# Kernel optimization log

Measured on AMD Instinct MI355X. Metric: run time of the kernel, lower is better.

## Reference

```python
import jax, jax.numpy as jnp
import numpy as np

B, N, DIM, HID = 128, 4096, 16, 128

def _linear_init(key, fan_in, fan_out):
    # torch nn.Linear default: U(-1/sqrt(fan_in), 1/sqrt(fan_in))
    kw, kb = jax.random.split(key)
    bound = 1.0 / np.sqrt(fan_in)
    W = jax.random.uniform(kw, (fan_in, fan_out), minval=-bound, maxval=bound, dtype=jnp.float32)
    b = jax.random.uniform(kb, (fan_out,), minval=-bound, maxval=bound, dtype=jnp.float32)
    return W, b

def setup_inputs() -> dict:
    key = jax.random.key(0)
    ks = jax.random.split(key, 8)
    x = jax.random.normal(ks[0], (B, N, DIM), dtype=jnp.float32)
    adj_col = (jax.random.uniform(ks[1], (N,), dtype=jnp.float32) > 0.5).astype(jnp.float32)
    W_n2e, b_n2e = _linear_init(ks[2], 2 * DIM, HID)
    W_e2e, b_e2e = _linear_init(ks[3], HID, HID)
    W_e2n, b_e2n = _linear_init(ks[4], HID, HID)
    W_n2n, b_n2n = _linear_init(ks[5], HID, HID)
    W_out, b_out = _linear_init(ks[6], DIM + HID, DIM)
    return {"x": x, "adj_col": adj_col,
            "W_n2e": W_n2e, "b_n2e": b_n2e,
            "W_e2e": W_e2e, "b_e2e": b_e2e,
            "W_e2n": W_e2n, "b_e2n": b_e2n,
            "W_n2n": W_n2n, "b_n2n": b_n2n,
            "W_out": W_out, "b_out": b_out,
            "i": 0}

def reference(x, adj_col, W_n2e, b_n2e, W_e2e, b_e2e, W_e2n, b_e2n, W_n2n, b_n2n, W_out, b_out, i):
    starter = x                                        # [B, N, dim]
    ender = x[:, i, :][:, None, :]                     # [B, 1, dim]
    ender = jnp.broadcast_to(ender, starter.shape)     # [B, N, dim]
    h = jnp.concatenate([starter, ender], axis=2)      # [B, N, 2*dim]
    h = jax.nn.relu(h @ W_n2e + b_n2e)                 # [B, N, hid]
    h = jax.nn.relu(h @ W_e2e + b_e2e)                 # [B, N, hid]
    h = h * adj_col[None, :, None]                     # adjacency mask
    h = jnp.sum(h, axis=1)                             # [B, hid]
    h = jax.nn.relu(h @ W_e2n + b_e2n)
    h = jax.nn.relu(h @ W_n2n + b_n2n)
    h = jnp.concatenate([starter[:, i, :], h], axis=-1)  # [B, dim+hid]
    return h @ W_out + b_out                           # [B, dim]
```

## Files before the change

### kernel.cpp

```cpp
#include <hip/hip_runtime.h>
#include <hip/hip_bf16.h>

#define B_    128
#define N_    4096
#define DIM_  16
#define HID_  128
#define NT_   2
#define ROWS_ (N_ / NT_)

typedef __bf16 bf16x2 __attribute__((ext_vector_type(2)));
typedef __bf16 bf16x8 __attribute__((ext_vector_type(8)));
typedef float floatx16 __attribute__((ext_vector_type(16)));
typedef unsigned int u32;
typedef unsigned int u32x4 __attribute__((ext_vector_type(4)));

__device__ inline bf16x8 load_cvt8(const float* __restrict__ p) {
  const float4 u = *(const float4*)p;
  const float4 v = *(const float4*)(p + 4);
  bf16x8 r;
  r[0] = (__bf16)u.x; r[1] = (__bf16)u.y; r[2] = (__bf16)u.z; r[3] = (__bf16)u.w;
  r[4] = (__bf16)v.x; r[5] = (__bf16)v.y; r[6] = (__bf16)v.z; r[7] = (__bf16)v.w;
  return r;
}

__device__ inline u32 pk2(float a, float b) {
  bf16x2 p; p[0] = (__bf16)a; p[1] = (__bf16)b;
  return __builtin_bit_cast(u32, p);
}

__global__ __launch_bounds__(256, 2) void edge_kernel(
    const float* __restrict__ x, const float* __restrict__ adj,
    const float* __restrict__ W1, const float* __restrict__ b1,
    const float* __restrict__ W2, const float* __restrict__ b2,
    const int* __restrict__ ip, float* __restrict__ part)
{
  __shared__ __align__(16) __bf16 sW2[HID_ * HID_];
  __shared__ int   sIdx[ROWS_ + 32];
  __shared__ float sAcc[HID_];
  __shared__ float sB1[HID_];
  __shared__ float sEnder[DIM_];
  __shared__ int   sCnt;

  const int t  = threadIdx.x;
  const int b  = blockIdx.y;
  const int n0 = blockIdx.x * ROWS_;
  const int ii = __ldg(ip);

  const int wave = t >> 6, lane = t & 63;
  const int half = lane >> 5, l31 = lane & 31;

  if (t == 0) sCnt = 0;
  if (t < HID_) sAcc[t] = 0.f;
  if (t < DIM_) sEnder[t] = x[((size_t)b * N_ + ii) * DIM_ + t];
  __syncthreads();

  #pragma unroll
  for (int r = t; r < ROWS_; r += 256) {
    const bool act = adj[n0 + r] != 0.f;
    const unsigned long long m = __ballot(act);
    int base = 0;
    if (lane == 0) base = atomicAdd(&sCnt, __popcll(m));
    base = __shfl(base, 0);
    if (act) {
      const int pre = __builtin_amdgcn_mbcnt_hi((u32)(m >> 32),
                      __builtin_amdgcn_mbcnt_lo((u32)m, 0));
      sIdx[base + pre] = n0 + r;
    }
  }

  #pragma unroll
  for (int e = 0; e < 8; ++e) {
    const int G = t * 8 + e;
    const int c = G >> 4, g = G & 15;
    bf16x8 v;
    #pragma unroll
    for (int j = 0; j < 8; ++j) v[j] = (__bf16)W2[((g << 3) + j) * HID_ + c];
    *(bf16x8*)&sW2[(c << 7) + ((g ^ (c & 15)) << 3)] = v;
  }

  bf16x8 w1f[4];
  #pragma unroll
  for (int ft = 0; ft < 4; ++ft) {
    bf16x8 v;
    #pragma unroll
    for (int j = 0; j < 8; ++j)
      v[j] = (__bf16)W1[(half * 8 + j) * HID_ + (ft * 32 + l31)];
    w1f[ft] = v;
  }

  if (t < HID_) {
    float s = b1[t];
    #pragma unroll
    for (int k = 0; k < DIM_; ++k) s += sEnder[k] * W1[(DIM_ + k) * HID_ + t];
    sB1[t] = s;
  }

  const float bv0 = b2[l31], bv1 = b2[32 + l31], bv2 = b2[64 + l31], bv3 = b2[96 + l31];

  __syncthreads();
  const int cnt = sCnt;
  const int nch = (cnt + 31) >> 5;
  for (int p = cnt + t; p < nch * 32; p += 256) sIdx[p] = n0;

  bf16x8 a2f[4], onef;
  #pragma unroll
  for (int j = 0; j < 8; ++j) onef[j] = (__bf16)0.f;
  if (half == 0) { onef[0] = (__bf16)1.f; onef[1] = (__bf16)1.f; }
  #pragma unroll
  for (int ft = 0; ft < 4; ++ft) {
    bf16x8 v;
    #pragma unroll
    for (int j = 0; j < 8; ++j) v[j] = (__bf16)0.f;
    if (half == 0) {
      const float s = sB1[ft * 32 + l31];
      const __bf16 hi = (__bf16)s;
      v[0] = hi;
      v[1] = (__bf16)(s - (float)hi);
    }
    a2f[ft] = v;
  }
  __syncthreads();

  float sum0 = 0.f, sum1 = 0.f, sum2 = 0.f, sum3 = 0.f;
  floatx16 zf;
  #pragma unroll
  for (int r = 0; r < 16; ++r) zf[r] = 0.f;

  for (int cb = wave * 32; cb < nch * 32; cb += 128) {
    const int row = sIdx[cb + l31];
    const bf16x8 xf = load_cvt8(&x[((size_t)b * N_ + row) * DIM_ + half * 8]);

    bf16x8 af[8];
    #pragma unroll
    for (int ft = 0; ft < 4; ++ft) {
      floatx16 hc = __builtin_amdgcn_mfma_f32_32x32x16_bf16(w1f[ft], xf, zf, 0, 0, 0);
      hc = __builtin_amdgcn_mfma_f32_32x32x16_bf16(a2f[ft], onef, hc, 0, 0, 0);
      #pragma unroll
      for (int sg = 0; sg < 2; ++sg) {
        float e0 = fmaxf(hc[8*sg+0], 0.f), e1 = fmaxf(hc[8*sg+1], 0.f);
        float e2 = fmaxf(hc[8*sg+2], 0.f), e3 = fmaxf(hc[8*sg+3], 0.f);
        float e4 = fmaxf(hc[8*sg+4], 0.f), e5 = fmaxf(hc[8*sg+5], 0.f);
        float e6 = fmaxf(hc[8*sg+6], 0.f), e7 = fmaxf(hc[8*sg+7], 0.f);
        const u32 lo0 = pk2(e0, e1), lo1 = pk2(e2, e3);
        const u32 hi0 = pk2(e4, e5), hi1 = pk2(e6, e7);
        const u32 sA = half ? lo0 : hi0;
        const u32 sB = half ? lo1 : hi1;
        const u32 rA = (u32)__shfl_xor((int)sA, 32);
        const u32 rB = (u32)__shfl_xor((int)sB, 32);
        u32x4 d;
        d[0] = half ? rA : lo0;
        d[1] = half ? rB : lo1;
        d[2] = half ? hi0 : rA;
        d[3] = half ? hi1 : rB;
        af[ft * 2 + sg] = __builtin_bit_cast(bf16x8, d);
      }
    }

    floatx16 c0 = zf, c1 = zf, c2 = zf, c3 = zf;
    #pragma unroll
    for (int s = 0; s < 8; ++s) {
      const int gp = ((s << 1) + half) ^ (l31 & 15);
      const __bf16* wp = &sW2[(l31 << 7) + (gp << 3)];
      const bf16x8 wb0 = *(const bf16x8*)(wp);
      const bf16x8 wb1 = *(const bf16x8*)(wp + (32 << 7));
      const bf16x8 wb2 = *(const bf16x8*)(wp + (64 << 7));
      const bf16x8 wb3 = *(const bf16x8*)(wp + (96 << 7));
      c0 = __builtin_amdgcn_mfma_f32_32x32x16_bf16(af[s], wb0, c0, 0, 0, 0);
      c1 = __builtin_amdgcn_mfma_f32_32x32x16_bf16(af[s], wb1, c1, 0, 0, 0);
      c2 = __builtin_amdgcn_mfma_f32_32x32x16_bf16(af[s], wb2, c2, 0, 0, 0);
      c3 = __builtin_amdgcn_mfma_f32_32x32x16_bf16(af[s], wb3, c3, 0, 0, 0);
    }

    if (cb + 32 <= cnt) {
      #pragma unroll
      for (int r = 0; r < 16; ++r) {
        sum0 += fmaxf(c0[r] + bv0, 0.f);
        sum1 += fmaxf(c1[r] + bv1, 0.f);
        sum2 += fmaxf(c2[r] + bv2, 0.f);
        sum3 += fmaxf(c3[r] + bv3, 0.f);
      }
    } else {
      #pragma unroll
      for (int r = 0; r < 16; ++r) {
        const int q = cb + (r & 3) + ((r >> 2) << 3) + (half << 2);
        if (q < cnt) {
          sum0 += fmaxf(c0[r] + bv0, 0.f);
          sum1 += fmaxf(c1[r] + bv1, 0.f);
          sum2 += fmaxf(c2[r] + bv2, 0.f);
          sum3 += fmaxf(c3[r] + bv3, 0.f);
        }
      }
    }
  }

  sum0 += __shfl_xor(sum0, 32);
  sum1 += __shfl_xor(sum1, 32);
  sum2 += __shfl_xor(sum2, 32);
  sum3 += __shfl_xor(sum3, 32);
  if (half == 0) {
    atomicAdd(&sAcc[l31],      sum0);
    atomicAdd(&sAcc[32 + l31], sum1);
    atomicAdd(&sAcc[64 + l31], sum2);
    atomicAdd(&sAcc[96 + l31], sum3);
  }
  __syncthreads();
  if (t < HID_) part[((size_t)b * NT_ + blockIdx.x) * HID_ + t] = sAcc[t];
}

__global__ void tail_kernel(
    const float* __restrict__ x, const float* __restrict__ part,
    const float* __restrict__ W3, const float* __restrict__ b3,
    const float* __restrict__ W4, const float* __restrict__ b4,
    const float* __restrict__ W5, const float* __restrict__ b5,
    const int* __restrict__ ip, float* __restrict__ out)
{
  const int b = blockIdx.x, t = threadIdx.x;
  __shared__ float s0[HID_], s1[HID_], s2[HID_], se[DIM_];
  const int ii = __ldg(ip);
  if (t < DIM_) se[t] = x[((size_t)b * N_ + ii) * DIM_ + t];
  float a = 0.f;
  #pragma unroll
  for (int p = 0; p < NT_; ++p) a += part[((size_t)b * NT_ + p) * HID_ + t];
  s0[t] = a;
  __syncthreads();
  float v = b3[t];
  #pragma unroll 16
  for (int k = 0; k < HID_; ++k) v += s0[k] * W3[k * HID_ + t];
  s1[t] = fmaxf(v, 0.f);
  __syncthreads();
  float w = b4[t];
  #pragma unroll 16
  for (int k = 0; k < HID_; ++k) w += s1[k] * W4[k * HID_ + t];
  s2[t] = fmaxf(w, 0.f);
  __syncthreads();
  if (t < DIM_) {
    float o = b5[t];
    #pragma unroll
    for (int k = 0; k < DIM_; ++k) o += se[k] * W5[k * DIM_ + t];
    #pragma unroll 16
    for (int k = 0; k < HID_; ++k) o += s2[k] * W5[(DIM_ + k) * DIM_ + t];
    out[b * DIM_ + t] = o;
  }
}

extern "C" void kernel_launch(void* const* d_in, const int* in_sizes, int n_in,
                              void* d_out, int out_size, void* d_ws, size_t ws_size,
                              hipStream_t stream) {
  const float* x   = (const float*)d_in[0];
  const float* adj = (const float*)d_in[1];
  const float* W1  = (const float*)d_in[2];
  const float* b1  = (const float*)d_in[3];
  const float* W2  = (const float*)d_in[4];
  const float* b2  = (const float*)d_in[5];
  const float* W3  = (const float*)d_in[6];
  const float* b3  = (const float*)d_in[7];
  const float* W4  = (const float*)d_in[8];
  const float* b4  = (const float*)d_in[9];
  const float* W5  = (const float*)d_in[10];
  const float* b5  = (const float*)d_in[11];
  const int*   ip  = (const int*)d_in[12];
  float* out  = (float*)d_out;
  float* part = (float*)d_ws;

  edge_kernel<<<dim3(NT_, B_), 256, 0, stream>>>(x, adj, W1, b1, W2, b2, ip, part);
  tail_kernel<<<B_, HID_, 0, stream>>>(x, part, W3, b3, W4, b4, W5, b5, ip, out);
}
```

Measured before the change: 133.3 us.

## Split output columns across wave pairs, raise grid tiling, prefetch next x rows

Each pair of waves now shares a 32-row chunk, and each wave computes half of the 128 output columns of the second layer, so accumulators are halved. The N dimension is split into 8 tiles instead of 2 and occupancy is raised to 4 blocks per CU, giving more blocks and more latency hiding. The x rows for the next chunk are loaded while the current one computes. In exchange, the first layer is recomputed redundantly by both waves of a pair, and the W2 shared-memory staging and bias setup are repeated in four times as many blocks.

```diff
diff --git a/kernel.cpp b/kernel.cpp
--- a/kernel.cpp
+++ b/kernel.cpp
@@ -5,7 +5,7 @@
 #define N_    4096
 #define DIM_  16
 #define HID_  128
-#define NT_   2
+#define NT_   8
 #define ROWS_ (N_ / NT_)
 
 typedef __bf16 bf16x2 __attribute__((ext_vector_type(2)));
@@ -28,14 +28,14 @@
   return __builtin_bit_cast(u32, p);
 }
 
-__global__ __launch_bounds__(256, 2) void edge_kernel(
+__global__ __launch_bounds__(256, 4) void edge_kernel(
     const float* __restrict__ x, const float* __restrict__ adj,
     const float* __restrict__ W1, const float* __restrict__ b1,
     const float* __restrict__ W2, const float* __restrict__ b2,
     const int* __restrict__ ip, float* __restrict__ part)
 {
   __shared__ __align__(16) __bf16 sW2[HID_ * HID_];
-  __shared__ int   sIdx[ROWS_ + 32];
+  __shared__ int   sIdx[ROWS_ + 128];
   __shared__ float sAcc[HID_];
   __shared__ float sB1[HID_];
   __shared__ float sEnder[DIM_];
@@ -48,6 +48,8 @@
 
   const int wave = t >> 6, lane = t & 63;
   const int half = lane >> 5, l31 = lane & 31;
+  const int g  = wave >> 1;
+  const int ch = wave & 1;
 
   if (t == 0) sCnt = 0;
   if (t < HID_) sAcc[t] = 0.f;
@@ -71,11 +73,11 @@
   #pragma unroll
   for (int e = 0; e < 8; ++e) {
     const int G = t * 8 + e;
-    const int c = G >> 4, g = G & 15;
+    const int c = G >> 4, gg = G & 15;
     bf16x8 v;
     #pragma unroll
-    for (int j = 0; j < 8; ++j) v[j] = (__bf16)W2[((g << 3) + j) * HID_ + c];
-    *(bf16x8*)&sW2[(c << 7) + ((g ^ (c & 15)) << 3)] = v;
+    for (int j = 0; j < 8; ++j) v[j] = (__bf16)W2[((gg << 3) + j) * HID_ + c];
+    *(bf16x8*)&sW2[(c << 7) + ((gg ^ (c & 15)) << 3)] = v;
   }
 
   bf16x8 w1f[4];
@@ -95,12 +97,13 @@
     sB1[t] = s;
   }
 
-  const float bv0 = b2[l31], bv1 = b2[32 + l31], bv2 = b2[64 + l31], bv3 = b2[96 + l31];
+  const float bv0 = b2[ch * 64 + l31], bv1 = b2[ch * 64 + 32 + l31];
 
   __syncthreads();
   const int cnt = sCnt;
-  const int nch = (cnt + 31) >> 5;
-  for (int p = cnt + t; p < nch * 32; p += 256) sIdx[p] = n0;
+  const int nch64 = (cnt + 63) >> 6;
+  const int end = nch64 * 64;
+  for (int p = cnt + t; p < end + 64; p += 256) sIdx[p] = n0;
 
   bf16x8 a2f[4], onef;
   #pragma unroll
@@ -121,14 +124,20 @@
   }
   __syncthreads();
 
-  float sum0 = 0.f, sum1 = 0.f, sum2 = 0.f, sum3 = 0.f;
+  float sum0 = 0.f, sum1 = 0.f;
   floatx16 zf;
   #pragma unroll
   for (int r = 0; r < 16; ++r) zf[r] = 0.f;
 
-  for (int cb = wave * 32; cb < nch * 32; cb += 128) {
+  int cb = g * 32;
+  bf16x8 xf;
+  {
     const int row = sIdx[cb + l31];
-    const bf16x8 xf = load_cvt8(&x[((size_t)b * N_ + row) * DIM_ + half * 8]);
+    xf = load_cvt8(&x[((size_t)b * N_ + row) * DIM_ + half * 8]);
+  }
+
+  for (; cb < end; cb += 64) {
+    const int nrow = sIdx[cb + 64 + l31];
 
     bf16x8 af[8];
     #pragma unroll
@@ -156,19 +165,17 @@
       }
     }
 
-    floatx16 c0 = zf, c1 = zf, c2 = zf, c3 = zf;
+    const bf16x8 nxf = load_cvt8(&x[((size_t)b * N_ + nrow) * DIM_ + half * 8]);
+
+    floatx16 c0 = zf, c1 = zf;
     #pragma unroll
     for (int s = 0; s < 8; ++s) {
       const int gp = ((s << 1) + half) ^ (l31 & 15);
-      const __bf16* wp = &sW2[(l31 << 7) + (gp << 3)];
+      const __bf16* wp = &sW2[((ch * 64 + l31) << 7) + (gp << 3)];
       const bf16x8 wb0 = *(const bf16x8*)(wp);
       const bf16x8 wb1 = *(const bf16x8*)(wp + (32 << 7));
-      const bf16x8 wb2 = *(const bf16x8*)(wp + (64 << 7));
-      const bf16x8 wb3 = *(const bf16x8*)(wp + (96 << 7));
       c0 = __builtin_amdgcn_mfma_f32_32x32x16_bf16(af[s], wb0, c0, 0, 0, 0);
       c1 = __builtin_amdgcn_mfma_f32_32x32x16_bf16(af[s], wb1, c1, 0, 0, 0);
-      c2 = __builtin_amdgcn_mfma_f32_32x32x16_bf16(af[s], wb2, c2, 0, 0, 0);
-      c3 = __builtin_amdgcn_mfma_f32_32x32x16_bf16(af[s], wb3, c3, 0, 0, 0);
     }
 
     if (cb + 32 <= cnt) {
@@ -176,8 +183,6 @@
       for (int r = 0; r < 16; ++r) {
         sum0 += fmaxf(c0[r] + bv0, 0.f);
         sum1 += fmaxf(c1[r] + bv1, 0.f);
-        sum2 += fmaxf(c2[r] + bv2, 0.f);
-        sum3 += fmaxf(c3[r] + bv3, 0.f);
       }
     } else {
       #pragma unroll
@@ -186,22 +191,17 @@
         if (q < cnt) {
           sum0 += fmaxf(c0[r] + bv0, 0.f);
           sum1 += fmaxf(c1[r] + bv1, 0.f);
-          sum2 += fmaxf(c2[r] + bv2, 0.f);
-          sum3 += fmaxf(c3[r] + bv3, 0.f);
         }
       }
     }
+    xf = nxf;
   }
 
   sum0 += __shfl_xor(sum0, 32);
   sum1 += __shfl_xor(sum1, 32);
-  sum2 += __shfl_xor(sum2, 32);
-  sum3 += __shfl_xor(sum3, 32);
   if (half == 0) {
-    atomicAdd(&sAcc[l31],      sum0);
-    atomicAdd(&sAcc[32 + l31], sum1);
-    atomicAdd(&sAcc[64 + l31], sum2);
-    atomicAdd(&sAcc[96 + l31], sum3);
+    atomicAdd(&sAcc[ch * 64 + l31],      sum0);
+    atomicAdd(&sAcc[ch * 64 + 32 + l31], sum1);
   }
   __syncthreads();
   if (t < HID_) part[((size_t)b * NT_ + blockIdx.x) * HID_ + t] = sAcc[t];
```

Result: slower. 165.0 us (+23.8%).
